# Kernel tuning notes

Hardware: AMD Instinct MI355X
Metric: run time of the kernel (lower is better)

The kernel has to match this reference:

```python
import jax, jax.numpy as jnp
from jax import lax
import numpy as np

E = 8       # num experts
TOP_K = 2   # top-k routing
H = 84      # moe hidden size


def _maxpool2(x):
    # 2x2 max pool, stride 2, NCHW
    return lax.reduce_window(x, -jnp.inf, lax.max, (1, 1, 2, 2), (1, 1, 2, 2), 'VALID')


def setup_inputs() -> dict:
    key = jax.random.key(0)
    ks = jax.random.split(key, 16)
    N = 16384
    def lin(k, out_d, in_d, scale=None):
        s = scale if scale is not None else 1.0 / np.sqrt(in_d)
        return jax.random.uniform(k, (out_d, in_d), jnp.float32, -s, s)
    inp = {
        'x': jax.random.normal(ks[0], (N, 3, 32, 32), jnp.float32),
        'conv1_w': jax.random.normal(ks[1], (6, 3, 5, 5), jnp.float32) * (1.0 / np.sqrt(3 * 25)),
        'conv1_b': jnp.zeros((6,), jnp.float32),
        'conv2_w': jax.random.normal(ks[2], (16, 6, 5, 5), jnp.float32) * (1.0 / np.sqrt(6 * 25)),
        'conv2_b': jnp.zeros((16,), jnp.float32),
        'fc1_w': lin(ks[3], 120, 400),
        'fc1_b': jnp.zeros((120,), jnp.float32),
        'fc2_w': lin(ks[4], H, 120),
        'fc2_b': jnp.zeros((H,), jnp.float32),
        'gate_w': jax.random.normal(ks[5], (H, E), jnp.float32) * 0.02,
        'expert_w': jax.random.normal(ks[6], (E, H, H), jnp.float32) * (1.0 / np.sqrt(H)),  # [E, out, in]
        'expert_b': jnp.zeros((E, H), jnp.float32),
        'head_w': lin(ks[7], 10, H),
        'head_b': jnp.zeros((10,), jnp.float32),
    }
    return inp


def _forward(x, conv1_w, conv1_b, conv2_w, conv2_b, fc1_w, fc1_b,
             fc2_w, fc2_b, gate_w, expert_w, expert_b, head_w, head_b):
    dn = ('NCHW', 'OIHW', 'NCHW')
    # LeNet feature extractor
    h = lax.conv_general_dilated(x, conv1_w, (1, 1), 'VALID', dimension_numbers=dn)
    h = jax.nn.relu(h + conv1_b[None, :, None, None])          # [N,6,28,28]
    h = _maxpool2(h)                                           # [N,6,14,14]
    h = lax.conv_general_dilated(h, conv2_w, (1, 1), 'VALID', dimension_numbers=dn)
    h = jax.nn.relu(h + conv2_b[None, :, None, None])          # [N,16,10,10]
    h = _maxpool2(h)                                           # [N,16,5,5]
    h = h.reshape(h.shape[0], -1)                              # [N,400]
    # MLP hiddens
    h = jax.nn.relu(h @ fc1_w.T + fc1_b)                       # [N,120]
    h = jax.nn.relu(h @ fc2_w.T + fc2_b)                       # [N,84]
    # MoE layer: top-k softmax gating, expert Linear(84,84), weighted combine
    logits = h @ gate_w                                        # [N,E]
    probs = jax.nn.softmax(logits, axis=-1)
    top_v, top_i = lax.top_k(probs, TOP_K)                     # [N,k]
    top_v = top_v / jnp.sum(top_v, axis=-1, keepdims=True)     # renormalize top-k gates
    N = h.shape[0]
    combine = jnp.zeros((N, E), h.dtype).at[jnp.arange(N)[:, None], top_i].add(top_v)  # [N,E]
    expert_out = jnp.einsum('nd,eod->neo', h, expert_w) + expert_b[None]               # [N,E,84]
    h = jnp.einsum('ne,neo->no', combine, expert_out)          # [N,84]
    # head
    return h @ head_w.T + head_b                               # [N,10]


def reference(x, conv1_w, conv1_b, conv2_w, conv2_b, fc1_w, fc1_b,
              fc2_w, fc2_b, gate_w, expert_w, expert_b, head_w, head_b):
    return _forward(x, conv1_w, conv1_b, conv2_w, conv2_b, fc1_w, fc1_b,
                    fc2_w, fc2_b, gate_w, expert_w, expert_b, head_w, head_b)
```

## Files before the change

kernel.cpp:

```cpp
#include <hip/hip_runtime.h>
#include <math.h>

typedef _Float16 half8 __attribute__((ext_vector_type(8)));
typedef float f32x4 __attribute__((ext_vector_type(4)));

__device__ inline uint splitpack(float v) {
    _Float16 h = (_Float16)v;
    float r = v - (float)h;
    _Float16 l = (_Float16)r;
    return (uint)__builtin_bit_cast(unsigned short, h) |
           ((uint)__builtin_bit_cast(unsigned short, l) << 16);
}
__device__ inline _Float16 lo16h(uint u) { return __builtin_bit_cast(_Float16, (unsigned short)(u & 0xffffu)); }
__device__ inline _Float16 hi16h(uint u) { return __builtin_bit_cast(_Float16, (unsigned short)(u >> 16)); }
__device__ inline uint packhh(_Float16 a, _Float16 b) {
    return (uint)__builtin_bit_cast(unsigned short, a) |
           ((uint)__builtin_bit_cast(unsigned short, b) << 16);
}
__device__ inline float dpp_max8(float v) {
    int x = __builtin_amdgcn_mov_dpp(__builtin_bit_cast(int, v), 0x128, 0xf, 0xf, true);
    return fmaxf(v, __builtin_bit_cast(float, x));
}

__global__ __launch_bounds__(256) void k_conv1(const float* __restrict__ x,
                                               const float* __restrict__ w,
                                               const float* __restrict__ b,
                                               uint* __restrict__ p1) {
    __shared__ uint simg[6720];
    const int tid  = threadIdx.x;
    const int lane = tid & 63;
    const int wv   = tid >> 6;
    const int n0   = blockIdx.x * 2;

    const int colb = lane & 15;
    const int c  = colb & 7, dx = colb >> 3;
    const int g  = lane >> 4;
    const int qr = g;

    half8 bh[3], bl[3];
    #pragma unroll
    for (int ks = 0; ks < 3; ++ks)
        #pragma unroll
        for (int jj = 0; jj < 8; ++jj) {
            int pi = jj >> 1, e = jj & 1;
            int rho = g * 4 + pi;
            float val = 0.f;
            if (rho < 15 && c < 6) {
                int ci = rho / 5, ky = rho % 5;
                int kx = ks * 2 + e - dx;
                if (kx >= 0 && kx < 5) val = w[c * 75 + ci * 25 + ky * 5 + kx];
            }
            _Float16 hh = (_Float16)val;
            bh[ks][jj] = hh;
            bl[ks][jj] = (_Float16)(val - (float)hh);
        }
    const float bias = (c < 6) ? b[c] : 0.f;

    for (int i = tid; i < 1536; i += 256) {
        int im = i / 768;
        int rem = i - im * 768;
        int plane = rem >> 8, rr = (rem & 255) >> 3, f = rem & 7;
        float4 v = *(const float4*)(x + ((size_t)(n0 + im) * 3 + plane) * 1024 + rr * 32 + f * 4);
        _Float16 h0 = (_Float16)v.x, h1 = (_Float16)v.y, h2 = (_Float16)v.z, h3 = (_Float16)v.w;
        _Float16 l0 = (_Float16)(v.x - (float)h0), l1 = (_Float16)(v.y - (float)h1);
        _Float16 l2 = (_Float16)(v.z - (float)h2), l3 = (_Float16)(v.w - (float)h3);
        int base = im * 3360 + plane * 1120 + rr * 35 + f * 2;
        simg[base]      = packhh(h0, h1);
        simg[base + 1]  = packhh(h2, h3);
        simg[base + 16] = packhh(l0, l1);
        simg[base + 17] = packhh(l2, l3);
    }
    __syncthreads();

    int poff[4];
    #pragma unroll
    for (int pi = 0; pi < 4; ++pi) {
        int rho = g * 4 + pi;
        if (rho > 14) rho = 14;
        poff[pi] = (rho / 5) * 1120 + (rho % 5) * 35;
    }

    for (int t0 = wv; t0 < 50; t0 += 8) {
        const int t1 = (t0 + 4 < 50) ? (t0 + 4) : t0;
        const int im0 = (t0 >= 25) ? 1 : 0, tl0 = t0 - im0 * 25;
        const int im1 = (t1 >= 25) ? 1 : 0, tl1 = t1 - im1 * 25;
        int r0c = tl0 * 16 + colb; if (r0c > 391) r0c = 391;
        int r1c = tl1 * 16 + colb; if (r1c > 391) r1c = 391;
        int qx0 = (r0c * 586) >> 14, yy0 = r0c - qx0 * 28;
        int qx1 = (r1c * 586) >> 14, yy1 = r1c - qx1 * 28;
        const uint* base0 = simg + im0 * 3360 + yy0 * 35 + qx0;
        const uint* base1 = simg + im1 * 3360 + yy1 * 35 + qx1;

        f32x4 A0[2] = {{0.f,0.f,0.f,0.f},{0.f,0.f,0.f,0.f}};
        f32x4 A1[2] = {{0.f,0.f,0.f,0.f},{0.f,0.f,0.f,0.f}};
        int c0 = 0, c1 = 0;
        #pragma unroll
        for (int ks = 0; ks < 3; ++ks) {
            uint h0[4], l0[4], h1[4], l1[4];
            #pragma unroll
            for (int pi = 0; pi < 4; ++pi) {
                const uint* a0p = base0 + poff[pi];
                const uint* a1p = base1 + poff[pi];
                h0[pi] = a0p[ks];  l0[pi] = a0p[16 + ks];
                h1[pi] = a1p[ks];  l1[pi] = a1p[16 + ks];
            }
            uint4 hv0; hv0.x = h0[0]; hv0.y = h0[1]; hv0.z = h0[2]; hv0.w = h0[3];
            uint4 lv0; lv0.x = l0[0]; lv0.y = l0[1]; lv0.z = l0[2]; lv0.w = l0[3];
            uint4 hv1; hv1.x = h1[0]; hv1.y = h1[1]; hv1.z = h1[2]; hv1.w = h1[3];
            uint4 lv1; lv1.x = l1[0]; lv1.y = l1[1]; lv1.z = l1[2]; lv1.w = l1[3];
            half8 ah0 = __builtin_bit_cast(half8, hv0);
            half8 al0 = __builtin_bit_cast(half8, lv0);
            half8 ah1 = __builtin_bit_cast(half8, hv1);
            half8 al1 = __builtin_bit_cast(half8, lv1);
            A0[c0 & 1] = __builtin_amdgcn_mfma_f32_16x16x32_f16(ah0, bh[ks], A0[c0 & 1], 0, 0, 0); ++c0;
            A1[c1 & 1] = __builtin_amdgcn_mfma_f32_16x16x32_f16(ah1, bh[ks], A1[c1 & 1], 0, 0, 0); ++c1;
            A0[c0 & 1] = __builtin_amdgcn_mfma_f32_16x16x32_f16(ah0, bl[ks], A0[c0 & 1], 0, 0, 0); ++c0;
            A1[c1 & 1] = __builtin_amdgcn_mfma_f32_16x16x32_f16(ah1, bl[ks], A1[c1 & 1], 0, 0, 0); ++c1;
            A0[c0 & 1] = __builtin_amdgcn_mfma_f32_16x16x32_f16(al0, bh[ks], A0[c0 & 1], 0, 0, 0); ++c0;
            A1[c1 & 1] = __builtin_amdgcn_mfma_f32_16x16x32_f16(al1, bh[ks], A1[c1 & 1], 0, 0, 0); ++c1;
        }
        {
            f32x4 acc;
            #pragma unroll
            for (int i = 0; i < 4; ++i) acc[i] = A0[0][i] + A0[1][i];
            float p01 = dpp_max8(fmaxf(acc[0], acc[1]));
            float p23 = dpp_max8(fmaxf(acc[2], acc[3]));
            if (dx == 0 && c < 6) {
                uint* outb = p1 + ((size_t)(n0 + im0) * 6 + c) * 196;
                int r0 = tl0 * 16 + qr * 4;
                if (r0 + 1 < 392) {
                    int qxa = (r0 * 586) >> 14, ya = r0 - qxa * 28;
                    outb[(ya >> 1) * 14 + qxa] = splitpack(fmaxf(p01 + bias, 0.f));
                }
                int r2 = r0 + 2;
                if (r2 + 1 < 392) {
                    int qxb = (r2 * 586) >> 14, yb = r2 - qxb * 28;
                    outb[(yb >> 1) * 14 + qxb] = splitpack(fmaxf(p23 + bias, 0.f));
                }
            }
        }
        if (t1 != t0) {
            f32x4 acc;
            #pragma unroll
            for (int i = 0; i < 4; ++i) acc[i] = A1[0][i] + A1[1][i];
            float p01 = dpp_max8(fmaxf(acc[0], acc[1]));
            float p23 = dpp_max8(fmaxf(acc[2], acc[3]));
            if (dx == 0 && c < 6) {
                uint* outb = p1 + ((size_t)(n0 + im1) * 6 + c) * 196;
                int r0 = tl1 * 16 + qr * 4;
                if (r0 + 1 < 392) {
                    int qxa = (r0 * 586) >> 14, ya = r0 - qxa * 28;
                    outb[(ya >> 1) * 14 + qxa] = splitpack(fmaxf(p01 + bias, 0.f));
                }
                int r2 = r0 + 2;
                if (r2 + 1 < 392) {
                    int qxb = (r2 * 586) >> 14, yb = r2 - qxb * 28;
                    outb[(yb >> 1) * 14 + qxb] = splitpack(fmaxf(p23 + bias, 0.f));
                }
            }
        }
    }
}

__global__ __launch_bounds__(256) void k_conv2(const uint* __restrict__ p1,
                                               const float* __restrict__ w,
                                               const float* __restrict__ b,
                                               float* __restrict__ p2) {
    __shared__ uint simg[4 * 1260];
    const int tid  = threadIdx.x;
    const int lane = tid & 63;
    const int wv   = tid >> 6;
    const int n0   = blockIdx.x * 4;
    const int g  = lane >> 4;
    const int cc = lane & 15;
    const int qr = g;

    for (int i = tid; i < 5040; i += 256) {
        int img = i / 1260, rem = i % 1260;
        int c = rem / 210, rr = rem % 210;
        int y = rr / 15, xx = rr % 15;
        uint v = 0u;
        if (xx < 14) v = p1[(size_t)(n0 + img) * 1176 + c * 196 + y * 14 + xx];
        simg[i] = v;
    }

    half8 bh[6], bl[6];
    #pragma unroll
    for (int ks = 0; ks < 6; ++ks)
        #pragma unroll
        for (int jj = 0; jj < 8; ++jj) {
            int pi = jj >> 1, e = jj & 1;
            int rho = (ks / 3) * 16 + g * 4 + pi;
            int kx = (ks % 3) * 2 + e;
            float val = 0.f;
            if (rho < 30 && kx < 5) {
                int ci = rho / 5, ky = rho % 5;
                val = w[cc * 150 + ci * 25 + ky * 5 + kx];
            }
            _Float16 hh = (_Float16)val;
            bh[ks][jj] = hh;
            bl[ks][jj] = (_Float16)(val - (float)hh);
        }
    const float bias = b[cc];
    __syncthreads();

    int poff2[8];
    #pragma unroll
    for (int sp = 0; sp < 8; ++sp) {
        int sel = sp >> 2, pi = sp & 3;
        int rho = sel * 16 + g * 4 + pi;
        if (rho > 29) rho = 29;
        poff2[sp] = (rho / 5) * 210 + (rho % 5) * 15;
    }

    const uint* img = simg + wv * 1260;
    const int qw  = (lane & 15) >> 2;
    const int dy  = (lane >> 1) & 1, dxx = lane & 1;
    float* outb = p2 + (size_t)(n0 + wv) * 400 + cc * 25;

    for (int t = 0; t < 7; ++t) {
        int qa = t * 4 + qw; if (qa > 24) qa = 24;
        int qy = qa / 5, qx = qa % 5;
        int base = (2 * qy + dy) * 15 + (2 * qx + dxx);
        f32x4 acc2[2] = {{0.f,0.f,0.f,0.f},{0.f,0.f,0.f,0.f}};
        int pp = 0;
        #pragma unroll
        for (int sel = 0; sel < 2; ++sel) {
            uint P[4][6];
            #pragma unroll
            for (int pi = 0; pi < 4; ++pi) {
                const uint* ap = img + base + poff2[sel * 4 + pi];
                #pragma unroll
                for (int k = 0; k < 6; ++k) P[pi][k] = ap[k];
            }
            #pragma unroll
            for (int ksr = 0; ksr < 3; ++ksr) {
                const int ks = sel * 3 + ksr;
                uint hu[4], lu[4];
                #pragma unroll
                for (int pi = 0; pi < 4; ++pi) {
                    uint d0 = P[pi][ksr * 2], d1 = P[pi][ksr * 2 + 1];
                    hu[pi] = __builtin_amdgcn_perm(d1, d0, 0x05040100u);
                    lu[pi] = __builtin_amdgcn_perm(d1, d0, 0x07060302u);
                }
                uint4 hv; hv.x = hu[0]; hv.y = hu[1]; hv.z = hu[2]; hv.w = hu[3];
                uint4 lv; lv.x = lu[0]; lv.y = lu[1]; lv.z = lu[2]; lv.w = lu[3];
                half8 ah = __builtin_bit_cast(half8, hv);
                half8 al = __builtin_bit_cast(half8, lv);
                acc2[pp & 1] = __builtin_amdgcn_mfma_f32_16x16x32_f16(ah, bh[ks], acc2[pp & 1], 0, 0, 0); ++pp;
                acc2[pp & 1] = __builtin_amdgcn_mfma_f32_16x16x32_f16(ah, bl[ks], acc2[pp & 1], 0, 0, 0); ++pp;
                acc2[pp & 1] = __builtin_amdgcn_mfma_f32_16x16x32_f16(al, bh[ks], acc2[pp & 1], 0, 0, 0); ++pp;
            }
        }
        int qc = t * 4 + qr;
        if (qc < 25) {
            float m = fmaxf(fmaxf(acc2[0][0] + acc2[1][0], acc2[0][1] + acc2[1][1]),
                            fmaxf(acc2[0][2] + acc2[1][2], acc2[0][3] + acc2[1][3]));
            outb[qc] = fmaxf(m + bias, 0.f);
        }
    }
}

__global__ __launch_bounds__(256) void k_compose(const float* __restrict__ ew,
                                                 const float* __restrict__ eb,
                                                 const float* __restrict__ hw,
                                                 float* __restrict__ C,
                                                 float* __restrict__ hb2) {
    __shared__ float shw[840];
    __shared__ float seb[672];
    const int e = blockIdx.x, tid = threadIdx.x;
    for (int i = tid; i < 840; i += 256) shw[i] = hw[i];
    for (int i = tid; i < 672; i += 256) seb[i] = eb[i];
    __syncthreads();
    for (int i = tid; i < 840; i += 256) {
        int o = i / 84, d = i % 84;
        float s = 0.f;
        for (int j = 0; j < 84; ++j)
            s = fmaf(shw[o * 84 + j], ew[((size_t)e * 84 + j) * 84 + d], s);
        C[e * 840 + i] = s;
    }
    if (tid < 10) {
        float s = 0.f;
        for (int j = 0; j < 84; ++j) s = fmaf(shw[tid * 84 + j], seb[e * 84 + j], s);
        hb2[e * 10 + tid] = s;
    }
}

__global__ __launch_bounds__(512) void k_fc1tail(const float* __restrict__ p2,
                                                 const float* __restrict__ f1w,
                                                 const float* __restrict__ f1b,
                                                 const float* __restrict__ f2w,
                                                 const float* __restrict__ f2b,
                                                 const float* __restrict__ gw,
                                                 const float* __restrict__ Cw,
                                                 const float* __restrict__ hb2,
                                                 const float* __restrict__ headb,
                                                 float* __restrict__ out) {
    __shared__ float region[23872];
    __shared__ float sh1[7680];
    __shared__ int   sei[128];
    const int tid = threadIdx.x;
    const int n0 = blockIdx.x * 64;

    {
        float* sa  = region;
        float* swt = region + 6400;
        const int tc = tid % 30, tr = tid / 30;
        float acc[8][4];
        #pragma unroll
        for (int i = 0; i < 8; ++i)
            #pragma unroll
            for (int j = 0; j < 4; ++j) acc[i][j] = 0.f;

        for (int kt = 0; kt < 4; ++kt) {
            __syncthreads();
            for (int i = tid; i < 1600; i += 512) {
                int r = i / 25, k4 = (i % 25) * 4;
                float4 v = *(const float4*)(p2 + (size_t)(n0 + r) * 400 + kt * 100 + k4);
                *(float4*)(sa + r * 100 + k4) = v;
            }
            for (int i = tid; i < 3000; i += 512) {
                int c = i / 25, k4 = (i % 25) * 4;
                float4 v = *(const float4*)(f1w + (size_t)c * 400 + kt * 100 + k4);
                float* d = swt + c * 101 + k4;
                d[0] = v.x; d[1] = v.y; d[2] = v.z; d[3] = v.w;
            }
            __syncthreads();
            if (tr < 8) {
                #pragma unroll 4
                for (int k = 0; k < 100; ++k) {
                    float av[8], wv[4];
                    #pragma unroll
                    for (int i = 0; i < 8; ++i) av[i] = sa[(tr * 8 + i) * 100 + k];
                    #pragma unroll
                    for (int j = 0; j < 4; ++j) wv[j] = swt[(tc * 4 + j) * 101 + k];
                    #pragma unroll
                    for (int i = 0; i < 8; ++i)
                        #pragma unroll
                        for (int j = 0; j < 4; ++j) acc[i][j] = fmaf(av[i], wv[j], acc[i][j]);
                }
            }
        }
        __syncthreads();
        if (tr < 8) {
            #pragma unroll
            for (int j = 0; j < 4; ++j) {
                const int o = tc * 4 + j;
                const float bo = f1b[o];
                #pragma unroll
                for (int i = 0; i < 8; ++i)
                    sh1[(tr * 8 + i) * 120 + o] = fmaxf(acc[i][j] + bo, 0.f);
            }
        }
    }

    float* sfw  = region;
    float* sC   = region + 10164;
    float* sh   = region + 16964;
    float* sgw  = region + 22404;
    float* shb2s= region + 23076;
    float* shb  = region + 23156;
    float* slog = region + 23168;
    float* swt2 = region + 23744;

    for (int i = tid; i < 2520; i += 512) {
        int o = i / 30, k4 = (i % 30) * 4;
        float4 v = *(const float4*)(f2w + (size_t)o * 120 + k4);
        float* d = sfw + o * 121 + k4;
        d[0] = v.x; d[1] = v.y; d[2] = v.z; d[3] = v.w;
    }
    for (int i = tid; i < 6720; i += 512) sC[(i / 84) * 85 + (i % 84)] = Cw[i];
    for (int i = tid; i < 672; i += 512) sgw[i] = gw[i];
    if (tid < 84) shb[100] = shb[100];
    if (tid < 80) shb2s[tid] = hb2[tid];
    if (tid < 10) shb[tid] = headb[tid];
    __shared__ float sfb[84];
    if (tid < 84) sfb[tid] = f2b[tid];
    __syncthreads();

    for (int i = tid; i < 5376; i += 512) {
        const int t = i / 84, o = i % 84;
        const float* a = sh1 + t * 120;
        const float* wr = sfw + o * 121;
        float s = 0.f;
        #pragma unroll 8
        for (int k = 0; k < 120; ++k) s = fmaf(a[k], wr[k], s);
        sh[t * 85 + o] = fmaxf(s + sfb[o], 0.f);
    }
    __syncthreads();

    {
        const int t = tid / 8, e = tid % 8;
        const float* a = sh + t * 85;
        float s = 0.f;
        #pragma unroll 4
        for (int d = 0; d < 84; ++d) s = fmaf(a[d], sgw[d * 8 + e], s);
        slog[t * 9 + e] = s;
    }
    __syncthreads();

    if (tid < 64) {
        const float* l = slog + tid * 9;
        float m1 = l[0]; int i1 = 0;
        #pragma unroll
        for (int e = 1; e < 8; ++e) if (l[e] > m1) { m1 = l[e]; i1 = e; }
        float m2 = -1e30f; int i2 = 0;
        #pragma unroll
        for (int e = 0; e < 8; ++e) if (e != i1 && l[e] > m2) { m2 = l[e]; i2 = e; }
        const float r = expf(m2 - m1);
        const float inv = 1.f / (1.f + r);
        swt2[tid * 2] = inv; swt2[tid * 2 + 1] = r * inv;
        sei[tid * 2] = i1; sei[tid * 2 + 1] = i2;
    }
    __syncthreads();

    for (int i = tid; i < 640; i += 512) {
        const int t = i / 10, o = i % 10;
        const float* a = sh + t * 85;
        const float w0 = swt2[t * 2], w1 = swt2[t * 2 + 1];
        const int e0 = sei[t * 2], e1 = sei[t * 2 + 1];
        const float* c0 = sC + (e0 * 10 + o) * 85;
        const float* c1 = sC + (e1 * 10 + o) * 85;
        float s0 = 0.f, s1 = 0.f;
        #pragma unroll 4
        for (int d = 0; d < 84; ++d) {
            s0 = fmaf(a[d], c0[d], s0);
            s1 = fmaf(a[d], c1[d], s1);
        }
        out[(size_t)(n0 + t) * 10 + o] =
            shb[o] + w0 * (s0 + shb2s[e0 * 10 + o]) + w1 * (s1 + shb2s[e1 * 10 + o]);
    }
}

extern "C" void kernel_launch(void* const* d_in, const int* in_sizes, int n_in,
                              void* d_out, int out_size, void* d_ws, size_t ws_size,
                              hipStream_t stream) {
    const float* x   = (const float*)d_in[0];
    const float* c1w = (const float*)d_in[1];
    const float* c1b = (const float*)d_in[2];
    const float* c2w = (const float*)d_in[3];
    const float* c2b = (const float*)d_in[4];
    const float* f1w = (const float*)d_in[5];
    const float* f1b = (const float*)d_in[6];
    const float* f2w = (const float*)d_in[7];
    const float* f2b = (const float*)d_in[8];
    const float* gw  = (const float*)d_in[9];
    const float* ew  = (const float*)d_in[10];
    const float* eb  = (const float*)d_in[11];
    const float* hw  = (const float*)d_in[12];
    const float* hb  = (const float*)d_in[13];
    float* out = (float*)d_out;

    const int N = in_sizes[0] / 3072;

    float* ws = (float*)d_ws;
    uint*  p1  = (uint*)ws;
    float* p2  = ws + (size_t)N * 1176;
    float* C   = p2 + (size_t)N * 400;
    float* hb2 = C + 6720;

    k_conv1<<<N / 2, 256, 0, stream>>>(x, c1w, c1b, p1);
    k_conv2<<<N / 4, 256, 0, stream>>>(p1, c2w, c2b, p2);
    k_compose<<<8, 256, 0, stream>>>(ew, eb, hw, C, hb2);
    k_fc1tail<<<N / 64, 512, 0, stream>>>(p2, f1w, f1b, f2w, f2b, gw, C, hb2, hb, out);
}
```

Measured before the change: 298.5 us.

## Store pooled conv1 output in padded layout, vectorize conv2 load, rebalance fc1 threads

conv1 now writes its pooled output straight into the padded 15-wide row layout that conv2 uses in shared memory, and zeros the pad column itself. conv2 can then fill shared memory with a plain uint4 bulk copy instead of a scalar gather with division and modulo. Separately, the fc1 tile in the tail kernel is remapped so nearly all 512 threads each compute a 4x4 block, instead of only 240 threads each computing an 8x4 block. In exchange the intermediate buffer grows slightly and conv1 performs extra global stores for the pad column.

New measurement: 294.0 us. About the same (-1.5%).

```diff
diff --git a/kernel.cpp b/kernel.cpp
--- a/kernel.cpp
+++ b/kernel.cpp
@@ -69,6 +69,11 @@
         simg[base + 1]  = packhh(h2, h3);
         simg[base + 16] = packhh(l0, l1);
         simg[base + 17] = packhh(l2, l3);
+    }
+    for (int i = tid; i < 168; i += 256) {
+        int im = i / 84, rem = i % 84;
+        int cc2 = rem / 14, y = rem % 14;
+        p1[(size_t)(n0 + im) * 1260 + cc2 * 210 + y * 15 + 14] = 0u;
     }
     __syncthreads();
 
@@ -126,16 +131,16 @@
             float p01 = dpp_max8(fmaxf(acc[0], acc[1]));
             float p23 = dpp_max8(fmaxf(acc[2], acc[3]));
             if (dx == 0 && c < 6) {
-                uint* outb = p1 + ((size_t)(n0 + im0) * 6 + c) * 196;
+                uint* outb = p1 + (size_t)(n0 + im0) * 1260 + c * 210;
                 int r0 = tl0 * 16 + qr * 4;
                 if (r0 + 1 < 392) {
                     int qxa = (r0 * 586) >> 14, ya = r0 - qxa * 28;
-                    outb[(ya >> 1) * 14 + qxa] = splitpack(fmaxf(p01 + bias, 0.f));
+                    outb[(ya >> 1) * 15 + qxa] = splitpack(fmaxf(p01 + bias, 0.f));
                 }
                 int r2 = r0 + 2;
                 if (r2 + 1 < 392) {
                     int qxb = (r2 * 586) >> 14, yb = r2 - qxb * 28;
-                    outb[(yb >> 1) * 14 + qxb] = splitpack(fmaxf(p23 + bias, 0.f));
+                    outb[(yb >> 1) * 15 + qxb] = splitpack(fmaxf(p23 + bias, 0.f));
                 }
             }
         }
@@ -146,16 +151,16 @@
             float p01 = dpp_max8(fmaxf(acc[0], acc[1]));
             float p23 = dpp_max8(fmaxf(acc[2], acc[3]));
             if (dx == 0 && c < 6) {
-                uint* outb = p1 + ((size_t)(n0 + im1) * 6 + c) * 196;
+                uint* outb = p1 + (size_t)(n0 + im1) * 1260 + c * 210;
                 int r0 = tl1 * 16 + qr * 4;
                 if (r0 + 1 < 392) {
                     int qxa = (r0 * 586) >> 14, ya = r0 - qxa * 28;
-                    outb[(ya >> 1) * 14 + qxa] = splitpack(fmaxf(p01 + bias, 0.f));
+                    outb[(ya >> 1) * 15 + qxa] = splitpack(fmaxf(p01 + bias, 0.f));
                 }
                 int r2 = r0 + 2;
                 if (r2 + 1 < 392) {
                     int qxb = (r2 * 586) >> 14, yb = r2 - qxb * 28;
-                    outb[(yb >> 1) * 14 + qxb] = splitpack(fmaxf(p23 + bias, 0.f));
+                    outb[(yb >> 1) * 15 + qxb] = splitpack(fmaxf(p23 + bias, 0.f));
                 }
             }
         }
@@ -166,7 +171,7 @@
                                                const float* __restrict__ w,
                                                const float* __restrict__ b,
                                                float* __restrict__ p2) {
-    __shared__ uint simg[4 * 1260];
+    __shared__ __align__(16) uint simg[4 * 1260];
     const int tid  = threadIdx.x;
     const int lane = tid & 63;
     const int wv   = tid >> 6;
@@ -175,13 +180,10 @@
     const int cc = lane & 15;
     const int qr = g;
 
-    for (int i = tid; i < 5040; i += 256) {
-        int img = i / 1260, rem = i % 1260;
-        int c = rem / 210, rr = rem % 210;
-        int y = rr / 15, xx = rr % 15;
-        uint v = 0u;
-        if (xx < 14) v = p1[(size_t)(n0 + img) * 1176 + c * 196 + y * 14 + xx];
-        simg[i] = v;
+    {
+        const uint4* pg = (const uint4*)(p1 + (size_t)n0 * 1260);
+        uint4* sg = (uint4*)simg;
+        for (int i = tid; i < 1260; i += 256) sg[i] = pg[i];
     }
 
     half8 bh[6], bl[6];
@@ -298,6 +300,7 @@
                                                  float* __restrict__ out) {
     __shared__ float region[23872];
     __shared__ float sh1[7680];
+    __shared__ float sfb[84];
     __shared__ int   sei[128];
     const int tid = threadIdx.x;
     const int n0 = blockIdx.x * 64;
@@ -305,10 +308,11 @@
     {
         float* sa  = region;
         float* swt = region + 6400;
-        const int tc = tid % 30, tr = tid / 30;
-        float acc[8][4];
-        #pragma unroll
-        for (int i = 0; i < 8; ++i)
+        const int rg = tid >> 5;
+        const int cg = tid & 31;
+        float acc[4][4];
+        #pragma unroll
+        for (int i = 0; i < 4; ++i)
             #pragma unroll
             for (int j = 0; j < 4; ++j) acc[i][j] = 0.f;
 
@@ -326,30 +330,30 @@
                 d[0] = v.x; d[1] = v.y; d[2] = v.z; d[3] = v.w;
             }
             __syncthreads();
-            if (tr < 8) {
+            if (cg < 30) {
                 #pragma unroll 4
                 for (int k = 0; k < 100; ++k) {
-                    float av[8], wv[4];
+                    float av[4], wv[4];
                     #pragma unroll
-                    for (int i = 0; i < 8; ++i) av[i] = sa[(tr * 8 + i) * 100 + k];
+                    for (int i = 0; i < 4; ++i) av[i] = sa[(rg * 4 + i) * 100 + k];
                     #pragma unroll
-                    for (int j = 0; j < 4; ++j) wv[j] = swt[(tc * 4 + j) * 101 + k];
+                    for (int j = 0; j < 4; ++j) wv[j] = swt[(cg * 4 + j) * 101 + k];
                     #pragma unroll
-                    for (int i = 0; i < 8; ++i)
+                    for (int i = 0; i < 4; ++i)
                         #pragma unroll
                         for (int j = 0; j < 4; ++j) acc[i][j] = fmaf(av[i], wv[j], acc[i][j]);
                 }
             }
         }
         __syncthreads();
-        if (tr < 8) {
+        if (cg < 30) {
             #pragma unroll
             for (int j = 0; j < 4; ++j) {
-                const int o = tc * 4 + j;
+                const int o = cg * 4 + j;
                 const float bo = f1b[o];
                 #pragma unroll
-                for (int i = 0; i < 8; ++i)
-                    sh1[(tr * 8 + i) * 120 + o] = fmaxf(acc[i][j] + bo, 0.f);
+                for (int i = 0; i < 4; ++i)
+                    sh1[(rg * 4 + i) * 120 + o] = fmaxf(acc[i][j] + bo, 0.f);
             }
         }
     }
@@ -371,10 +375,8 @@
     }
     for (int i = tid; i < 6720; i += 512) sC[(i / 84) * 85 + (i % 84)] = Cw[i];
     for (int i = tid; i < 672; i += 512) sgw[i] = gw[i];
-    if (tid < 84) shb[100] = shb[100];
     if (tid < 80) shb2s[tid] = hb2[tid];
     if (tid < 10) shb[tid] = headb[tid];
-    __shared__ float sfb[84];
     if (tid < 84) sfb[tid] = f2b[tid];
     __syncthreads();
 
@@ -455,7 +457,7 @@
 
     float* ws = (float*)d_ws;
     uint*  p1  = (uint*)ws;
-    float* p2  = ws + (size_t)N * 1176;
+    float* p2  = ws + (size_t)N * 1260;
     float* C   = p2 + (size_t)N * 400;
     float* hb2 = C + 6720;
 
```
